# Optimization experiments

Measured on AMD Instinct MI355X. Metric: run time of the kernel, lower is better.

Reference implementation:

```python
import jax, jax.numpy as jnp
import numpy as np
from jax import lax

RADIUS = 0.3
NSAMPLE = 16
NPOINT = 1024
NH = 1   # num_heading_bin
NS = 18  # num_size_cluster
EPS = 1e-5  # torch BatchNorm eps


def _bn(x, g, b, m, v):
    # eval-mode batchnorm over the last (channel) axis
    return (x - m) * (g / jnp.sqrt(v + EPS)) + b


def _fps(xyz, npoint):
    # furthest point sampling; xyz: (B,K,3) -> (B,npoint) int32 indices
    B, K, _ = xyz.shape
    def body(carry, _):
        dists, far = carry
        cur = jnp.take_along_axis(xyz, far[:, None, None], axis=1)  # (B,1,3)
        d = jnp.sum((xyz - cur) ** 2, -1)                           # (B,K)
        dists = jnp.minimum(dists, d)
        nxt = jnp.argmax(dists, -1).astype(jnp.int32)
        return (dists, nxt), far
    init = (jnp.full((B, K), 1e10, xyz.dtype), jnp.zeros((B,), jnp.int32))
    _, inds = lax.scan(body, init, None, length=npoint)
    return jnp.swapaxes(inds, 0, 1)  # (B, npoint)


def _ball_query(xyz, new_xyz):
    # first-NSAMPLE points within RADIUS of each center, pad with first hit
    K = xyz.shape[1]
    d2 = jnp.sum((new_xyz[:, :, None, :] - xyz[:, None, :, :]) ** 2, -1)  # (B,S,K)
    mask = d2 < RADIUS ** 2
    idx = jnp.where(mask, jnp.arange(K, dtype=jnp.int32)[None, None, :], K)
    idx = jnp.sort(idx, -1)[..., :NSAMPLE]
    first = idx[..., :1]
    idx = jnp.where(idx == K, first, idx)
    idx = jnp.where(idx == K, 0, idx)  # degenerate: no neighbor at all
    return idx  # (B,S,NSAMPLE)


def setup_inputs() -> dict:
    key = jax.random.key(0)
    ks = jax.random.split(key, 32)
    inp = {}
    inp['xyz'] = jax.random.normal(ks[0], (8, 8192, 3), jnp.float32)
    inp['features'] = jax.random.normal(ks[1], (8, 256, 8192), jnp.float32)
    i = 2
    # shared MLP: 259 -> 128 -> 128 -> 128 (conv2d 1x1, no bias, then BN)
    for l, (o, c) in enumerate([(128, 259), (128, 128), (128, 128)]):
        inp[f'mlp_w{l}'] = jax.random.normal(ks[i], (o, c), jnp.float32) * 0.1; i += 1
        inp[f'mlp_g{l}'] = jnp.ones((o,), jnp.float32)
        inp[f'mlp_b{l}'] = jnp.zeros((o,), jnp.float32)
        inp[f'mlp_m{l}'] = jax.random.normal(ks[i], (o,), jnp.float32) * 0.01; i += 1
        inp[f'mlp_v{l}'] = jax.random.uniform(ks[i], (o,), jnp.float32, 0.5, 1.5); i += 1
    # box head convs (conv1d k=1)
    for nm, (o, c) in [('c1', (128, 128)), ('c2', (128, 128)), ('c3', (97, 128))]:
        inp[f'{nm}_w'] = jax.random.normal(ks[i], (o, c), jnp.float32) * 0.1; i += 1
        inp[f'{nm}_b'] = jnp.zeros((o,), jnp.float32)
    for nm in ['bn1', 'bn2']:
        inp[f'{nm}_g'] = jnp.ones((128,), jnp.float32)
        inp[f'{nm}_b'] = jnp.zeros((128,), jnp.float32)
        inp[f'{nm}_m'] = jax.random.normal(ks[i], (128,), jnp.float32) * 0.01; i += 1
        inp[f'{nm}_v'] = jax.random.uniform(ks[i], (128,), jnp.float32, 0.5, 1.5); i += 1
    inp['mean_size_arr'] = jax.random.uniform(ks[i], (NS, 3), jnp.float32, 0.3, 2.0)
    return inp


def reference(xyz, features,
              mlp_w0, mlp_g0, mlp_b0, mlp_m0, mlp_v0,
              mlp_w1, mlp_g1, mlp_b1, mlp_m1, mlp_v1,
              mlp_w2, mlp_g2, mlp_b2, mlp_m2, mlp_v2,
              c1_w, c1_b, bn1_g, bn1_b, bn1_m, bn1_v,
              c2_w, c2_b, bn2_g, bn2_b, bn2_m, bn2_v,
              c3_w, c3_b, mean_size_arr):
    B = xyz.shape[0]
    # --- vote aggregation: FPS + ball query + group + shared MLP + maxpool ---
    fps_inds = _fps(xyz, NPOINT)
    new_xyz = jnp.take_along_axis(xyz, fps_inds[..., None], axis=1)  # (B,S,3)
    idx = _ball_query(xyz, new_xyz)                                  # (B,S,n)
    gather = jax.vmap(lambda a, i: a[i])
    g_xyz = (gather(xyz, idx) - new_xyz[:, :, None, :]) / RADIUS     # normalize_xyz
    g_f = gather(jnp.swapaxes(features, 1, 2), idx)                  # (B,S,n,256)
    h = jnp.concatenate([g_xyz, g_f], -1)                            # (B,S,n,259)
    for w, g, b, m, v in ((mlp_w0, mlp_g0, mlp_b0, mlp_m0, mlp_v0),
                          (mlp_w1, mlp_g1, mlp_b1, mlp_m1, mlp_v1),
                          (mlp_w2, mlp_g2, mlp_b2, mlp_m2, mlp_v2)):
        h = jax.nn.relu(_bn(jnp.einsum('bsnc,oc->bsno', h, w), g, b, m, v))
    feat = jnp.max(h, axis=2)                                        # (B,S,128)
    # --- box head (conv1d k=1 == per-point linear) ---
    net = jax.nn.relu(_bn(jnp.einsum('bsc,oc->bso', feat, c1_w) + c1_b,
                          bn1_g, bn1_b, bn1_m, bn1_v))
    net = jax.nn.relu(_bn(jnp.einsum('bsc,oc->bso', net, c2_w) + c2_b,
                          bn2_g, bn2_b, bn2_m, bn2_v))
    net = jnp.einsum('bsc,oc->bso', net, c3_w) + c3_b                # (B,S,97)
    # --- decode_scores ---
    obj = net[..., 0:2]
    center = new_xyz + net[..., 2:5]
    hs = net[..., 5:5 + NH]
    hr = net[..., 5 + NH:5 + 2 * NH] * (np.pi / NH)
    ss = net[..., 5 + 2 * NH:5 + 2 * NH + NS]
    srn = net[..., 5 + 2 * NH + NS:5 + 2 * NH + 4 * NS].reshape(B, NPOINT, NS, 3)
    sr = (srn * mean_size_arr[None, None]).reshape(B, NPOINT, NS * 3)
    sem = net[..., 5 + 2 * NH + 4 * NS:]
    return jnp.concatenate([obj, center, hs, hr, ss, sr, sem], -1)   # (B,S,97)
```

## Files before the change

### kernel.cpp

```cpp
#include <hip/hip_runtime.h>
#include <cstdint>
#include <cstddef>

#define BATCH   8
#define KPTS    8192
#define NPT     1024
#define NSAMP   16
#define RAD2    0.09f

typedef float f32x2 __attribute__((ext_vector_type(2)));

template <int CTRL>
__device__ __forceinline__ unsigned long long dpp_max_step(unsigned long long v) {
    unsigned int lo = (unsigned int)v, hi = (unsigned int)(v >> 32);
    unsigned int lo2 = (unsigned int)__builtin_amdgcn_update_dpp(0, (int)lo, CTRL, 0xf, 0xf, true);
    unsigned int hi2 = (unsigned int)__builtin_amdgcn_update_dpp(0, (int)hi, CTRL, 0xf, 0xf, true);
    unsigned long long o = ((unsigned long long)hi2 << 32) | lo2;
    return o > v ? o : v;
}

__global__ __launch_bounds__(512, 1) void fps_f0_kernel(
    const float* __restrict__ xyz, float* __restrict__ new_xyz,
    const float* __restrict__ feats, const float* __restrict__ w0,
    float* __restrict__ f0out) {
    __shared__ float xs[KPTS], ys[KPTS], zs[KPTS];
    __shared__ __align__(16) unsigned long long wslot[2][8];
    __shared__ int   hist[NPT];
    __shared__ float As[16 * 128];
    __shared__ float Bs[16 * 130];

    const int tid = threadIdx.x;

    if (blockIdx.x >= 8) {
        const int bid = blockIdx.x - 8;
        const int b   = bid >> 6;
        const int p0  = (bid & 63) << 7;
        const int rb  = (tid >> 4) << 2;
        const int ob  = tid & 15;
        const float* fb = feats + (size_t)b * 256 * KPTS;

        float acc[4][8];
#pragma unroll
        for (int r = 0; r < 4; ++r)
#pragma unroll
            for (int c = 0; c < 8; ++c) acc[r][c] = 0.f;

        for (int k0 = 0; k0 < 256; k0 += 16) {
#pragma unroll
            for (int i = 0; i < 4; ++i) {
                int e = tid + (i << 9);
                int kk = e >> 7, pc = e & 127;
                As[kk * 128 + pc] = fb[(size_t)(k0 + kk) * KPTS + p0 + pc];
            }
#pragma unroll
            for (int i = 0; i < 4; ++i) {
                int e = tid + (i << 9);
                int o = e >> 4, kk = e & 15;
                Bs[kk * 130 + o] = w0[o * 259 + 3 + k0 + kk];
            }
            __syncthreads();
#pragma unroll
            for (int kk = 0; kk < 16; ++kk) {
                float a[4], wvv[8];
#pragma unroll
                for (int r = 0; r < 4; ++r) a[r] = As[kk * 128 + rb + r];
#pragma unroll
                for (int c = 0; c < 8; ++c) wvv[c] = Bs[kk * 130 + ob + (c << 4)];
#pragma unroll
                for (int r = 0; r < 4; ++r)
#pragma unroll
                    for (int c = 0; c < 8; ++c) acc[r][c] = fmaf(a[r], wvv[c], acc[r][c]);
            }
            __syncthreads();
        }
#pragma unroll
        for (int r = 0; r < 4; ++r) {
            float* outp = f0out + ((size_t)b * KPTS + p0 + rb + r) * 128 + ob;
#pragma unroll
            for (int c = 0; c < 8; ++c) outp[c << 4] = acc[r][c];
        }
        return;
    }

    {
#pragma clang fp contract(off)
        const int b = blockIdx.x;
        const float* xb = xyz + (size_t)b * KPTS * 3;

        for (int i = tid; i < KPTS; i += 512) {
            xs[i] = xb[i * 3 + 0];
            ys[i] = xb[i * 3 + 1];
            zs[i] = xb[i * 3 + 2];
        }
        __syncthreads();

        const int base = tid << 4;
        f32x2 px[8], py[8], pz[8], dmn[8];
#pragma unroll
        for (int j = 0; j < 8; ++j) {
            int i0 = base + (j << 1);
            px[j] = (f32x2){xs[i0], xs[i0 + 1]};
            py[j] = (f32x2){ys[i0], ys[i0 + 1]};
            pz[j] = (f32x2){zs[i0], zs[i0 + 1]};
            dmn[j] = (f32x2){1e10f, 1e10f};
        }

        int far = 0;
        for (int it = 0; it < NPT; ++it) {
            if (tid == 0) hist[it] = far;
            const float cx = xs[far], cy = ys[far], cz = zs[far];
            const f32x2 cx2 = (f32x2){cx, cx};
            const f32x2 cy2 = (f32x2){cy, cy};
            const f32x2 cz2 = (f32x2){cz, cz};

            f32x2 mm = (f32x2){-1.0f, -1.0f};
#pragma unroll
            for (int j = 0; j < 8; ++j) {
                f32x2 dx = px[j] - cx2;
                f32x2 dy = py[j] - cy2;
                f32x2 dz = pz[j] - cz2;
                f32x2 d  = (dx * dx + dy * dy) + dz * dz;
                f32x2 nd = __builtin_elementwise_min(dmn[j], d);
                dmn[j] = nd;
                mm = __builtin_elementwise_max(mm, nd);
            }
            float lmax = fmaxf(mm.x, mm.y);

            int ci = 0x7fffffff;
#pragma unroll
            for (int j = 0; j < 8; ++j) {
                if (dmn[j].x == lmax) ci = min(ci, base + (j << 1));
                if (dmn[j].y == lmax) ci = min(ci, base + (j << 1) + 1);
            }

            unsigned long long pk =
                ((unsigned long long)__float_as_uint(lmax) << 32) | (unsigned)(8191 - ci);

            pk = dpp_max_step<0x111>(pk);
            pk = dpp_max_step<0x112>(pk);
            pk = dpp_max_step<0x114>(pk);
            pk = dpp_max_step<0x118>(pk);
            pk = dpp_max_step<0x142>(pk);
            pk = dpp_max_step<0x143>(pk);

            if ((tid & 63) == 63) wslot[it & 1][tid >> 6] = pk;
            __syncthreads();

            ulonglong2 s01 = *(const ulonglong2*)&wslot[it & 1][0];
            ulonglong2 s23 = *(const ulonglong2*)&wslot[it & 1][2];
            ulonglong2 s45 = *(const ulonglong2*)&wslot[it & 1][4];
            ulonglong2 s67 = *(const ulonglong2*)&wslot[it & 1][6];
            unsigned long long g = s01.x;
            if (s01.y > g) g = s01.y;
            if (s23.x > g) g = s23.x;
            if (s23.y > g) g = s23.y;
            if (s45.x > g) g = s45.x;
            if (s45.y > g) g = s45.y;
            if (s67.x > g) g = s67.x;
            if (s67.y > g) g = s67.y;
            far = 8191 - (int)(unsigned)(g & 0xffffffffull);
        }

        for (int i = tid; i < NPT; i += 512) {
            int idx = hist[i];
            float* o = new_xyz + ((size_t)b * NPT + i) * 3;
            o[0] = xs[idx]; o[1] = ys[idx]; o[2] = zs[idx];
        }
    }
}

__global__ __launch_bounds__(256) void ballq_kernel(const float* __restrict__ xyz,
                                                    const float* __restrict__ new_xyz,
                                                    int* __restrict__ idxout) {
    const int tid  = threadIdx.x;
    const int lane = tid & 63;
    const int q    = (blockIdx.x << 2) + (tid >> 6);
    const int b    = q >> 10;
    const float* xb = xyz + (size_t)b * KPTS * 3;
    const float qx = new_xyz[q * 3 + 0];
    const float qy = new_xyz[q * 3 + 1];
    const float qz = new_xyz[q * 3 + 2];
    int* op = idxout + q * NSAMP;

    int total = 0;
    int first_p = 0;
    for (int c = 0; c < KPTS / 64; ++c) {
        int p = (c << 6) + lane;
        float pxv = xb[p * 3 + 0], pyv = xb[p * 3 + 1], pzv = xb[p * 3 + 2];
        float dx = __fsub_rn(qx, pxv), dy = __fsub_rn(qy, pyv), dz = __fsub_rn(qz, pzv);
        float d2 = __fadd_rn(__fadd_rn(__fmul_rn(dx, dx), __fmul_rn(dy, dy)),
                             __fmul_rn(dz, dz));
        bool pred = d2 < RAD2;
        unsigned long long mask = __ballot(pred);
        if (total == 0 && mask != 0ull) first_p = (c << 6) + (int)__builtin_ctzll(mask);
        if (pred) {
            int rank = (int)__popcll(mask & ((1ull << lane) - 1ull));
            int slot = total + rank;
            if (slot < NSAMP) op[slot] = p;
        }
        total += (int)__popcll(mask);
        if (total >= NSAMP) break;
    }
    if (total < NSAMP && lane >= total && lane < NSAMP) op[lane] = first_p;
}

#define HS 129

__global__ __launch_bounds__(256) void mlp_kernel(
    const float* __restrict__ f0, const int* __restrict__ idxw,
    const float* __restrict__ xyz, const float* __restrict__ new_xyz,
    const float* __restrict__ w0,
    const float* __restrict__ g0, const float* __restrict__ b0,
    const float* __restrict__ m0, const float* __restrict__ v0,
    const float* __restrict__ w1,
    const float* __restrict__ g1, const float* __restrict__ b1a,
    const float* __restrict__ m1, const float* __restrict__ v1,
    const float* __restrict__ w2,
    const float* __restrict__ g2, const float* __restrict__ b2a,
    const float* __restrict__ m2, const float* __restrict__ v2,
    float* __restrict__ featout) {
    const int tid = threadIdx.x;
    const int q0  = blockIdx.x << 2;
    const int b   = q0 >> 10;

    __shared__ float h[64 * HS];
    __shared__ float Wsh[16 * HS];
    __shared__ float gx[64], gy[64], gz[64];
    __shared__ int   pidx[64];
    __shared__ float s0[128], t0[128], wxs[128], wys[128], wzs[128];
    __shared__ float s1[128], t1[128], s2[128], t2[128];

    if (tid < 64) pidx[tid] = idxw[(q0 + (tid >> 4)) * NSAMP + (tid & 15)];
    if (tid < 128) {
        float sc = g0[tid] / sqrtf(v0[tid] + 1e-5f);
        s0[tid] = sc; t0[tid] = b0[tid] - m0[tid] * sc;
        sc = g1[tid] / sqrtf(v1[tid] + 1e-5f);
        s1[tid] = sc; t1[tid] = b1a[tid] - m1[tid] * sc;
        sc = g2[tid] / sqrtf(v2[tid] + 1e-5f);
        s2[tid] = sc; t2[tid] = b2a[tid] - m2[tid] * sc;
        wxs[tid] = w0[tid * 259 + 0];
        wys[tid] = w0[tid * 259 + 1];
        wzs[tid] = w0[tid * 259 + 2];
    }
    __syncthreads();
    if (tid < 64) {
        int p = pidx[tid];
        int q = q0 + (tid >> 4);
        const float* pp = xyz + ((size_t)b * KPTS + p) * 3;
        const float* nq = new_xyz + (size_t)q * 3;
        gx[tid] = (pp[0] - nq[0]) / 0.3f;
        gy[tid] = (pp[1] - nq[1]) / 0.3f;
        gz[tid] = (pp[2] - nq[2]) / 0.3f;
    }
    __syncthreads();

#pragma unroll 4
    for (int i = 0; i < 32; ++i) {
        int e = tid + (i << 8);
        int row = e >> 7, o = e & 127;
        int p = pidx[row];
        float v = f0[((size_t)b * KPTS + p) * 128 + o];
        v = fmaf(wxs[o], gx[row], v);
        v = fmaf(wys[o], gy[row], v);
        v = fmaf(wzs[o], gz[row], v);
        v = fmaf(v, s0[o], t0[o]);
        h[row * HS + o] = fmaxf(v, 0.f);
    }
    __syncthreads();

    const int rb = (tid >> 4) << 2;
    const int ob = tid & 15;
    for (int layer = 0; layer < 2; ++layer) {
        const float* wmat = (layer == 0) ? w1 : w2;
        const float* ssp  = (layer == 0) ? s1 : s2;
        const float* ttp  = (layer == 0) ? t1 : t2;
        float acc[4][8];
#pragma unroll
        for (int r = 0; r < 4; ++r)
#pragma unroll
            for (int c = 0; c < 8; ++c) acc[r][c] = 0.f;

        for (int k0 = 0; k0 < 128; k0 += 16) {
#pragma unroll
            for (int i = 0; i < 8; ++i) {
                int e = tid + (i << 8);
                int o = e >> 4, kk = e & 15;
                Wsh[kk * HS + o] = wmat[o * 128 + k0 + kk];
            }
            __syncthreads();
#pragma unroll
            for (int kk = 0; kk < 16; ++kk) {
                float a[4], wvv[8];
#pragma unroll
                for (int r = 0; r < 4; ++r) a[r] = h[(rb + r) * HS + k0 + kk];
#pragma unroll
                for (int c = 0; c < 8; ++c) wvv[c] = Wsh[kk * HS + ob + (c << 4)];
#pragma unroll
                for (int r = 0; r < 4; ++r)
#pragma unroll
                    for (int c = 0; c < 8; ++c) acc[r][c] = fmaf(a[r], wvv[c], acc[r][c]);
            }
            __syncthreads();
        }
#pragma unroll
        for (int r = 0; r < 4; ++r)
#pragma unroll
            for (int c = 0; c < 8; ++c) {
                int o = ob + (c << 4);
                float v = fmaf(acc[r][c], ssp[o], ttp[o]);
                h[(rb + r) * HS + o] = fmaxf(v, 0.f);
            }
        __syncthreads();
    }

#pragma unroll
    for (int i = 0; i < 2; ++i) {
        int e = tid + (i << 8);
        int qq = e >> 7, o = e & 127;
        float m = h[(qq * 16) * HS + o];
#pragma unroll
        for (int n = 1; n < 16; ++n) m = fmaxf(m, h[(qq * 16 + n) * HS + o]);
        featout[(size_t)(q0 + qq) * 128 + o] = m;
    }
}

__global__ __launch_bounds__(256) void head_kernel(
    const float* __restrict__ feat, const float* __restrict__ new_xyz,
    const float* __restrict__ c1w, const float* __restrict__ c1b,
    const float* __restrict__ c2w, const float* __restrict__ c2b,
    const float* __restrict__ c3w, const float* __restrict__ c3b,
    const float* __restrict__ bg1, const float* __restrict__ bb1,
    const float* __restrict__ bm1, const float* __restrict__ bv1,
    const float* __restrict__ bg2, const float* __restrict__ bb2,
    const float* __restrict__ bm2, const float* __restrict__ bv2,
    const float* __restrict__ msz, float* __restrict__ out) {
    const int tid = threadIdx.x;
    const int q0  = blockIdx.x << 3;
    __shared__ float fs[8][128], n1[8][128], n2[8][128];
    __shared__ float s1[128], t1[128], s2[128], t2[128], ms[54];

#pragma unroll
    for (int i = 0; i < 4; ++i) {
        int e = tid + (i << 8);
        fs[e >> 7][e & 127] = feat[(size_t)q0 * 128 + e];
    }
    if (tid < 128) {
        float sc = bg1[tid] / sqrtf(bv1[tid] + 1e-5f);
        s1[tid] = sc; t1[tid] = bb1[tid] - bm1[tid] * sc;
        sc = bg2[tid] / sqrtf(bv2[tid] + 1e-5f);
        s2[tid] = sc; t2[tid] = bb2[tid] - bm2[tid] * sc;
    }
    if (tid < 54) ms[tid] = msz[tid];
    __syncthreads();

    const int o    = tid & 127;
    const int half = tid >> 7;

    {
        float a[4];
#pragma unroll
        for (int j = 0; j < 4; ++j) a[j] = c1b[o];
        const float* wr = c1w + o * 128;
        for (int k = 0; k < 128; k += 4) {
            float4 w4 = *(const float4*)(wr + k);
#pragma unroll
            for (int j = 0; j < 4; ++j) {
                int qq = half * 4 + j;
                a[j] = fmaf(fs[qq][k + 0], w4.x, a[j]);
                a[j] = fmaf(fs[qq][k + 1], w4.y, a[j]);
                a[j] = fmaf(fs[qq][k + 2], w4.z, a[j]);
                a[j] = fmaf(fs[qq][k + 3], w4.w, a[j]);
            }
        }
#pragma unroll
        for (int j = 0; j < 4; ++j)
            n1[half * 4 + j][o] = fmaxf(fmaf(a[j], s1[o], t1[o]), 0.f);
    }
    __syncthreads();
    {
        float a[4];
#pragma unroll
        for (int j = 0; j < 4; ++j) a[j] = c2b[o];
        const float* wr = c2w + o * 128;
        for (int k = 0; k < 128; k += 4) {
            float4 w4 = *(const float4*)(wr + k);
#pragma unroll
            for (int j = 0; j < 4; ++j) {
                int qq = half * 4 + j;
                a[j] = fmaf(n1[qq][k + 0], w4.x, a[j]);
                a[j] = fmaf(n1[qq][k + 1], w4.y, a[j]);
                a[j] = fmaf(n1[qq][k + 2], w4.z, a[j]);
                a[j] = fmaf(n1[qq][k + 3], w4.w, a[j]);
            }
        }
#pragma unroll
        for (int j = 0; j < 4; ++j)
            n2[half * 4 + j][o] = fmaxf(fmaf(a[j], s2[o], t2[o]), 0.f);
    }
    __syncthreads();
    if (o < 97) {
        float a[4];
#pragma unroll
        for (int j = 0; j < 4; ++j) a[j] = c3b[o];
        const float* wr = c3w + o * 128;
        for (int k = 0; k < 128; k += 4) {
            float4 w4 = *(const float4*)(wr + k);
#pragma unroll
            for (int j = 0; j < 4; ++j) {
                int qq = half * 4 + j;
                a[j] = fmaf(n2[qq][k + 0], w4.x, a[j]);
                a[j] = fmaf(n2[qq][k + 1], w4.y, a[j]);
                a[j] = fmaf(n2[qq][k + 2], w4.z, a[j]);
                a[j] = fmaf(n2[qq][k + 3], w4.w, a[j]);
            }
        }
#pragma unroll
        for (int j = 0; j < 4; ++j) {
            int q = q0 + half * 4 + j;
            float v = a[j];
            if (o >= 2 && o < 5) v += new_xyz[(size_t)q * 3 + (o - 2)];
            else if (o == 6) v *= 3.14159265358979323846f;
            else if (o >= 25 && o < 79) v *= ms[o - 25];
            out[(size_t)q * 97 + o] = v;
        }
    }
}

extern "C" void kernel_launch(void* const* d_in, const int* in_sizes, int n_in,
                              void* d_out, int out_size, void* d_ws, size_t ws_size,
                              hipStream_t stream) {
    const float* xyz      = (const float*)d_in[0];
    const float* features = (const float*)d_in[1];
    const float* w0  = (const float*)d_in[2];
    const float* g0  = (const float*)d_in[3];
    const float* b0  = (const float*)d_in[4];
    const float* m0  = (const float*)d_in[5];
    const float* v0  = (const float*)d_in[6];
    const float* w1  = (const float*)d_in[7];
    const float* g1  = (const float*)d_in[8];
    const float* b1  = (const float*)d_in[9];
    const float* m1  = (const float*)d_in[10];
    const float* v1  = (const float*)d_in[11];
    const float* w2  = (const float*)d_in[12];
    const float* g2  = (const float*)d_in[13];
    const float* b2  = (const float*)d_in[14];
    const float* m2  = (const float*)d_in[15];
    const float* v2  = (const float*)d_in[16];
    const float* c1w = (const float*)d_in[17];
    const float* c1b = (const float*)d_in[18];
    const float* c2w = (const float*)d_in[19];
    const float* c2b = (const float*)d_in[20];
    const float* c3w = (const float*)d_in[21];
    const float* c3b = (const float*)d_in[22];
    const float* bg1 = (const float*)d_in[23];
    const float* bb1 = (const float*)d_in[24];
    const float* bm1 = (const float*)d_in[25];
    const float* bv1 = (const float*)d_in[26];
    const float* bg2 = (const float*)d_in[27];
    const float* bb2 = (const float*)d_in[28];
    const float* bm2 = (const float*)d_in[29];
    const float* bv2 = (const float*)d_in[30];
    const float* msz = (const float*)d_in[31];

    float* F0   = (float*)d_ws;
    float* feat = F0 + (size_t)BATCH * KPTS * 128;
    int*   idxw = (int*)(feat + (size_t)BATCH * NPT * 128);
    float* nxyz = (float*)(idxw + (size_t)BATCH * NPT * NSAMP);
    float* outp = (float*)d_out;

    fps_f0_kernel<<<8 + BATCH * (KPTS / 128), 512, 0, stream>>>(
        xyz, nxyz, features, w0, F0);
    ballq_kernel<<<BATCH * NPT / 4, 256, 0, stream>>>(xyz, nxyz, idxw);
    mlp_kernel  <<<BATCH * NPT / 4, 256, 0, stream>>>(
        F0, idxw, xyz, nxyz, w0, g0, b0, m0, v0,
        w1, g1, b1, m1, v1, w2, g2, b2, m2, v2, feat);
    head_kernel <<<BATCH * NPT / 8, 256, 0, stream>>>(
        feat, nxyz, c1w, c1b, c2w, c2b, c3w, c3b,
        bg1, bb1, bm1, bv1, bg2, bb2, bm2, bv2, msz, outp);
}
```

Measured before the change: 1.424 ms.

## Run MLP layers 1-2 on bf16 MFMA with shuffle-based max pooling

The two 128x128 shared-MLP layers in mlp_kernel move from scalar fp32 FMA loops to bf16 MFMA 16x16x32 instructions. Each wave handles one center's 16 samples, and the full weight matrix is staged once in LDS as bf16 instead of in k-chunks. The layer-0 gather now uses float4 loads and writes bf16 activations. The max over samples becomes a per-lane reduction plus cross-lane shuffles, which drops the separate shared-memory pooling pass. Rounding activations and weights to bf16 lowers precision compared with the fp32 reference.

Result: faster. 1.252 ms (-12.0%).

```diff
diff --git a/kernel.cpp b/kernel.cpp
--- a/kernel.cpp
+++ b/kernel.cpp
@@ -9,6 +9,14 @@
 #define RAD2    0.09f
 
 typedef float f32x2 __attribute__((ext_vector_type(2)));
+typedef float f32x4 __attribute__((ext_vector_type(4)));
+typedef short s16x4 __attribute__((ext_vector_type(4)));
+typedef short s16x8 __attribute__((ext_vector_type(8)));
+
+__device__ __forceinline__ unsigned short f2bf(float x) {
+    unsigned u = __float_as_uint(x);
+    return (unsigned short)((u + 0x7fffu + ((u >> 16) & 1u)) >> 16);
+}
 
 template <int CTRL>
 __device__ __forceinline__ unsigned long long dpp_max_step(unsigned long long v) {
@@ -204,7 +212,7 @@
     if (total < NSAMP && lane >= total && lane < NSAMP) op[lane] = first_p;
 }
 
-#define HS 129
+#define HB 136
 
 __global__ __launch_bounds__(256) void mlp_kernel(
     const float* __restrict__ f0, const int* __restrict__ idxw,
@@ -223,8 +231,8 @@
     const int q0  = blockIdx.x << 2;
     const int b   = q0 >> 10;
 
-    __shared__ float h[64 * HS];
-    __shared__ float Wsh[16 * HS];
+    __shared__ __align__(16) unsigned short hbf[64 * HB];
+    __shared__ __align__(16) unsigned short Wsh[128 * HB];
     __shared__ float gx[64], gy[64], gz[64];
     __shared__ int   pidx[64];
     __shared__ float s0[128], t0[128], wxs[128], wys[128], wzs[128];
@@ -254,73 +262,103 @@
     }
     __syncthreads();
 
+#pragma unroll 2
+    for (int i = 0; i < 8; ++i) {
+        int e = tid + (i << 8);
+        int row = e >> 5, o = (e & 31) << 2;
+        int p = pidx[row];
+        float4 v4 = *(const float4*)(f0 + ((size_t)b * KPTS + p) * 128 + o);
+        float gxr = gx[row], gyr = gy[row], gzr = gz[row];
+        float r0 = fmaf(wzs[o + 0], gzr, fmaf(wys[o + 0], gyr, fmaf(wxs[o + 0], gxr, v4.x)));
+        float r1 = fmaf(wzs[o + 1], gzr, fmaf(wys[o + 1], gyr, fmaf(wxs[o + 1], gxr, v4.y)));
+        float r2 = fmaf(wzs[o + 2], gzr, fmaf(wys[o + 2], gyr, fmaf(wxs[o + 2], gxr, v4.z)));
+        float r3 = fmaf(wzs[o + 3], gzr, fmaf(wys[o + 3], gyr, fmaf(wxs[o + 3], gxr, v4.w)));
+        s16x4 c4;
+        c4.x = (short)f2bf(fmaxf(fmaf(r0, s0[o + 0], t0[o + 0]), 0.f));
+        c4.y = (short)f2bf(fmaxf(fmaf(r1, s0[o + 1], t0[o + 1]), 0.f));
+        c4.z = (short)f2bf(fmaxf(fmaf(r2, s0[o + 2], t0[o + 2]), 0.f));
+        c4.w = (short)f2bf(fmaxf(fmaf(r3, s0[o + 3], t0[o + 3]), 0.f));
+        *(s16x4*)&hbf[row * HB + o] = c4;
+    }
 #pragma unroll 4
-    for (int i = 0; i < 32; ++i) {
+    for (int i = 0; i < 16; ++i) {
         int e = tid + (i << 8);
-        int row = e >> 7, o = e & 127;
-        int p = pidx[row];
-        float v = f0[((size_t)b * KPTS + p) * 128 + o];
-        v = fmaf(wxs[o], gx[row], v);
-        v = fmaf(wys[o], gy[row], v);
-        v = fmaf(wzs[o], gz[row], v);
-        v = fmaf(v, s0[o], t0[o]);
-        h[row * HS + o] = fmaxf(v, 0.f);
-    }
-    __syncthreads();
-
-    const int rb = (tid >> 4) << 2;
-    const int ob = tid & 15;
-    for (int layer = 0; layer < 2; ++layer) {
-        const float* wmat = (layer == 0) ? w1 : w2;
-        const float* ssp  = (layer == 0) ? s1 : s2;
-        const float* ttp  = (layer == 0) ? t1 : t2;
-        float acc[4][8];
-#pragma unroll
-        for (int r = 0; r < 4; ++r)
-#pragma unroll
-            for (int c = 0; c < 8; ++c) acc[r][c] = 0.f;
-
-        for (int k0 = 0; k0 < 128; k0 += 16) {
-#pragma unroll
-            for (int i = 0; i < 8; ++i) {
-                int e = tid + (i << 8);
-                int o = e >> 4, kk = e & 15;
-                Wsh[kk * HS + o] = wmat[o * 128 + k0 + kk];
-            }
-            __syncthreads();
-#pragma unroll
-            for (int kk = 0; kk < 16; ++kk) {
-                float a[4], wvv[8];
-#pragma unroll
-                for (int r = 0; r < 4; ++r) a[r] = h[(rb + r) * HS + k0 + kk];
-#pragma unroll
-                for (int c = 0; c < 8; ++c) wvv[c] = Wsh[kk * HS + ob + (c << 4)];
-#pragma unroll
-                for (int r = 0; r < 4; ++r)
-#pragma unroll
-                    for (int c = 0; c < 8; ++c) acc[r][c] = fmaf(a[r], wvv[c], acc[r][c]);
-            }
-            __syncthreads();
-        }
-#pragma unroll
-        for (int r = 0; r < 4; ++r)
-#pragma unroll
-            for (int c = 0; c < 8; ++c) {
-                int o = ob + (c << 4);
-                float v = fmaf(acc[r][c], ssp[o], ttp[o]);
-                h[(rb + r) * HS + o] = fmaxf(v, 0.f);
-            }
-        __syncthreads();
-    }
-
-#pragma unroll
-    for (int i = 0; i < 2; ++i) {
+        int o = e >> 5;
+        int kt = (e & 31) << 2;
+        float4 w4 = *(const float4*)(w1 + o * 128 + kt);
+        s16x4 c4 = { (short)f2bf(w4.x), (short)f2bf(w4.y),
+                     (short)f2bf(w4.z), (short)f2bf(w4.w) };
+        *(s16x4*)&Wsh[o * HB + kt] = c4;
+    }
+    __syncthreads();
+
+    const int w    = tid >> 6;
+    const int lane = tid & 63;
+    const int l15  = lane & 15;
+    const int quad = lane >> 4;
+    const int wrow = w << 4;
+
+    f32x4 acc[8];
+#pragma unroll
+    for (int t = 0; t < 8; ++t) acc[t] = (f32x4){0.f, 0.f, 0.f, 0.f};
+#pragma unroll
+    for (int k0 = 0; k0 < 128; k0 += 32) {
+        s16x8 a = *(const s16x8*)&hbf[(wrow + l15) * HB + k0 + (quad << 3)];
+#pragma unroll
+        for (int t = 0; t < 8; ++t) {
+            s16x8 bf = *(const s16x8*)&Wsh[((t << 4) + l15) * HB + k0 + (quad << 3)];
+            acc[t] = __builtin_amdgcn_mfma_f32_16x16x32_bf16(a, bf, acc[t], 0, 0, 0);
+        }
+    }
+    __syncthreads();
+
+#pragma unroll
+    for (int t = 0; t < 8; ++t) {
+        int o = (t << 4) + l15;
+        float ss = s1[o], tt = t1[o];
+#pragma unroll
+        for (int r = 0; r < 4; ++r) {
+            float v = fmaxf(fmaf(acc[t][r], ss, tt), 0.f);
+            hbf[(wrow + (quad << 2) + r) * HB + o] = f2bf(v);
+        }
+    }
+#pragma unroll 4
+    for (int i = 0; i < 16; ++i) {
         int e = tid + (i << 8);
-        int qq = e >> 7, o = e & 127;
-        float m = h[(qq * 16) * HS + o];
-#pragma unroll
-        for (int n = 1; n < 16; ++n) m = fmaxf(m, h[(qq * 16 + n) * HS + o]);
-        featout[(size_t)(q0 + qq) * 128 + o] = m;
+        int o = e >> 5;
+        int kt = (e & 31) << 2;
+        float4 w4 = *(const float4*)(w2 + o * 128 + kt);
+        s16x4 c4 = { (short)f2bf(w4.x), (short)f2bf(w4.y),
+                     (short)f2bf(w4.z), (short)f2bf(w4.w) };
+        *(s16x4*)&Wsh[o * HB + kt] = c4;
+    }
+    __syncthreads();
+
+#pragma unroll
+    for (int t = 0; t < 8; ++t) acc[t] = (f32x4){0.f, 0.f, 0.f, 0.f};
+#pragma unroll
+    for (int k0 = 0; k0 < 128; k0 += 32) {
+        s16x8 a = *(const s16x8*)&hbf[(wrow + l15) * HB + k0 + (quad << 3)];
+#pragma unroll
+        for (int t = 0; t < 8; ++t) {
+            s16x8 bf = *(const s16x8*)&Wsh[((t << 4) + l15) * HB + k0 + (quad << 3)];
+            acc[t] = __builtin_amdgcn_mfma_f32_16x16x32_bf16(a, bf, acc[t], 0, 0, 0);
+        }
+    }
+
+#pragma unroll
+    for (int t = 0; t < 8; ++t) {
+        int o = (t << 4) + l15;
+        float ss = s2[o], tt = t2[o];
+        float m0v = fmaxf(fmaf(acc[t][0], ss, tt), 0.f);
+        float m1v = fmaxf(fmaf(acc[t][1], ss, tt), 0.f);
+        float m2v = fmaxf(fmaf(acc[t][2], ss, tt), 0.f);
+        float m3v = fmaxf(fmaf(acc[t][3], ss, tt), 0.f);
+        float m = fmaxf(fmaxf(m0v, m1v), fmaxf(m2v, m3v));
+        m = fmaxf(m, __shfl_xor(m, 16));
+        m = fmaxf(m, __shfl_xor(m, 32));
+        if (quad == 0)
+            featout[(size_t)(q0 + w) * 128 + o] = m;
     }
 }
 
```
